# Performance work log

Measured on AMD Instinct MI355X. Metric: run time of the kernel, lower is better.

Reference implementation:

```python
import jax, jax.numpy as jnp
import numpy as np

CONV_KERNEL_MAX_DIFF = 0.7  # self.conv_kernel_max_diff
PRE_KERNEL_MULT = 1.0       # self.pre_conv_kernel_mult


def setup_inputs() -> dict:
    B, C, N, K = 8, 64, 32, 3
    key = jax.random.key(0)
    k1, k2, k3 = jax.random.split(key, 3)
    conv_in = jax.random.normal(k1, (B, C, N, N), dtype=jnp.float32)
    pre_kernel = jax.random.normal(k2, (B, C, C, K, K), dtype=jnp.float32)
    bias = jax.random.normal(k3, (B, C, 1, 1), dtype=jnp.float32)
    return {"conv_in": conv_in, "pre_kernel": pre_kernel, "bias": bias}


def _identity_kernel(c, k, dtype):
    # 1 at the spatial center for matching in/out channel -> identity circular conv
    idx = jnp.arange(c)
    return jnp.zeros((c, c, k, k), dtype=dtype).at[idx, idx, k // 2, k // 2].set(1.0)


def reference(conv_in, pre_kernel, bias):
    B, C, N, _ = conv_in.shape
    Kk = pre_kernel.shape[-1]
    # K = 0.7 * tanh(pre_kernel) + I
    Kmat = CONV_KERNEL_MAX_DIFF * jnp.tanh(PRE_KERNEL_MULT * pre_kernel)
    Kmat = Kmat + _identity_kernel(C, Kk, conv_in.dtype)[None]
    # Embed k x k kernel into n x n with the center tap at the origin
    # (so the identity kernel acts as the identity map under circular conv).
    Kpad = jnp.zeros((B, C, C, N, N), dtype=conv_in.dtype).at[..., :Kk, :Kk].set(Kmat)
    Kpad = jnp.roll(Kpad, shift=(-(Kk // 2), -(Kk // 2)), axis=(-2, -1))
    # Circular conv2D diagonalizes per-frequency into c x c complex matrices.
    K_hat = jnp.fft.fft2(Kpad)            # [B,C,C,N,N] complex
    x_hat = jnp.fft.fft2(conv_in)         # [B,C,N,N] complex
    y_hat = jnp.einsum('boiuv,biuv->bouv', K_hat, x_hat)
    conv_out = jnp.real(jnp.fft.ifft2(y_hat)) + bias
    # log|det| of the block-circulant operator = sum over frequencies of
    # log|det K_hat[:, :, u, v]| (Schur-complement recursion in the original).
    mats = jnp.transpose(K_hat, (0, 3, 4, 1, 2))  # [B,N,N,C,C]
    _, logabsdet = jnp.linalg.slogdet(mats)
    logdet = jnp.sum(logabsdet, axis=(1, 2))      # [B]
    return conv_out, logdet
```

## Files before the change

kernel.cpp:

```cpp
#include <hip/hip_runtime.h>
#include <math.h>

#define BB 8
#define CC 64
#define NN 32
#define CONV_TOTAL (BB*CC*NN*NN)
#define KM_ELEMS (BB*9*CC*CC)
#define NCANON 514

typedef float v2f __attribute__((ext_vector_type(2)));

#define RL(x, l) __uint_as_float(__builtin_amdgcn_readlane(__float_as_uint(x), (l)))

__global__ __launch_bounds__(256) void build_km(const float* __restrict__ pre,
                                                float* __restrict__ km,
                                                float* __restrict__ logdet_out) {
    int idx = blockIdx.x * 256 + threadIdx.x;
    if (blockIdx.x == 0 && threadIdx.x < BB) logdet_out[threadIdx.x] = 0.f;
    if (idx >= KM_ELEMS) return;
    int b   = idx / (9 * 4096);
    int rem = idx - b * (9 * 4096);
    int j   = rem >> 12;
    int e   = rem & 4095;
    int o = e >> 6, i = e & 63;
    float v = 0.7f * tanhf(pre[(b * 4096 + e) * 9 + j]);
    if (o == i && j == 4) v += 1.0f;
    km[idx] = v;
}

__global__ __launch_bounds__(256) void conv_kernel(const float* __restrict__ x,
                                                   const float* __restrict__ km,
                                                   const float* __restrict__ bias,
                                                   float* __restrict__ out) {
    int b = blockIdx.x >> 6, o = blockIdx.x & 63;
    __shared__ float Kms[9][64];
    __shared__ float xs[1024];
    int t = threadIdx.x;
    for (int s = t; s < 576; s += 256) {
        int j = s >> 6, i = s & 63;
        Kms[j][i] = km[(b * 9 + j) * 4096 + (o << 6) + i];
    }
    float bb = bias[(b << 6) + o];
    float acc0 = bb, acc1 = bb, acc2 = bb, acc3 = bb;
    int u = t >> 3, v0 = (t & 7) << 2;
    const float* xb = x + (size_t)(b << 6) * 1024;
    for (int i = 0; i < 64; ++i) {
        float4 xv4 = *(const float4*)(xb + i * 1024 + (t << 2));
        __syncthreads();
        *(float4*)&xs[t << 2] = xv4;
        __syncthreads();
        #pragma unroll
        for (int dy = 0; dy < 3; ++dy) {
            int row = (u + 1 - dy) & 31;
            const float* xr = &xs[row << 5];
            float xv[6];
            #pragma unroll
            for (int q = 0; q < 6; ++q) xv[q] = xr[(v0 - 1 + q) & 31];
            #pragma unroll
            for (int dx = 0; dx < 3; ++dx) {
                float w = Kms[dy * 3 + dx][i];
                acc0 += w * xv[2 - dx];
                acc1 += w * xv[3 - dx];
                acc2 += w * xv[4 - dx];
                acc3 += w * xv[5 - dx];
            }
        }
    }
    float4 r = make_float4(acc0, acc1, acc2, acc3);
    *(float4*)(out + ((size_t)blockIdx.x << 10) + (u << 5) + v0) = r;
}

template<int K>
__device__ __forceinline__ void lu_steps(v2f (&A)[64], int lane, float &logsum) {
    float px = RL(A[K].x, K), py = RL(A[K].y, K);
    float mag = fmaf(px, px, py * py);
    logsum += 0.5f * __logf(mag);
    if constexpr (K < 63) {
        float inv = __builtin_amdgcn_rcpf(mag);
        float ax = A[K].x, ay = A[K].y;
        float mr = (ax * px + ay * py) * inv;
        float mi = (ay * px - ax * py) * inv;
        bool act = lane > K;
        mr = act ? mr : 0.f;
        mi = act ? mi : 0.f;
        v2f m1 = (v2f){-mr, -mr};
        v2f m2 = (v2f){ mi, -mi};
        #pragma unroll
        for (int c = K + 1; c < 64; ++c) {
            float pcx = RL(A[c].x, K), pcy = RL(A[c].y, K);
            v2f p1 = (v2f){pcx, pcy};
            v2f p2 = (v2f){pcy, pcx};
            A[c] = m1 * p1 + A[c];
            A[c] = m2 * p2 + A[c];
        }
        lu_steps<K + 1>(A, lane, logsum);
    }
}

__global__ __launch_bounds__(64, 1) void logdet_kernel(const float* __restrict__ km,
                                                       float* __restrict__ logdet_out) {
    int gid = blockIdx.x;
    int b = gid / NCANON, ci = gid - b * NCANON;
    int u, v;
    if (ci < 17)        { u = 0;                  v = ci; }
    else if (ci < 497)  { int r = ci - 17; u = 1 + (r >> 5); v = r & 31; }
    else                { u = 16;                 v = ci - 497; }
    float wgt = ((u == 0 || u == 16) && (v == 0 || v == 16)) ? 1.0f : 2.0f;

    int lane = threadIdx.x;

    v2f A[64];
    #pragma unroll
    for (int c = 0; c < 64; ++c) A[c] = (v2f){0.f, 0.f};

    const float* Kb = km + (size_t)b * 36864 + (lane << 6);
    #pragma unroll
    for (int j = 0; j < 9; ++j) {
        int dy = j / 3, dx = j % 3;
        float argrev = -(float)(u * (dy - 1) + v * (dx - 1)) * (1.0f / 32.0f);
        argrev = argrev - floorf(argrev);
        float cs = __builtin_amdgcn_cosf(argrev);
        float sn = __builtin_amdgcn_sinf(argrev);
        v2f csn = (v2f){cs, sn};
        const float* p = Kb + (j << 12);
        #pragma unroll
        for (int ch = 0; ch < 8; ++ch) {
            float4 k0 = *(const float4*)(p + (ch << 3) + 0);
            float4 k1 = *(const float4*)(p + (ch << 3) + 4);
            A[(ch << 3) + 0] += csn * k0.x;  A[(ch << 3) + 1] += csn * k0.y;
            A[(ch << 3) + 2] += csn * k0.z;  A[(ch << 3) + 3] += csn * k0.w;
            A[(ch << 3) + 4] += csn * k1.x;  A[(ch << 3) + 5] += csn * k1.y;
            A[(ch << 3) + 6] += csn * k1.z;  A[(ch << 3) + 7] += csn * k1.w;
            __builtin_amdgcn_sched_barrier(0);
        }
    }

    float logsum = 0.f;
    lu_steps<0>(A, lane, logsum);

    if (lane == 0) atomicAdd(&logdet_out[b], wgt * logsum);
}

extern "C" void kernel_launch(void* const* d_in, const int* in_sizes, int n_in,
                              void* d_out, int out_size, void* d_ws, size_t ws_size,
                              hipStream_t stream) {
    const float* conv_in    = (const float*)d_in[0];
    const float* pre_kernel = (const float*)d_in[1];
    const float* bias       = (const float*)d_in[2];
    float* out = (float*)d_out;
    float* km  = (float*)d_ws;
    float* logdet_out = out + CONV_TOTAL;

    build_km<<<KM_ELEMS / 256, 256, 0, stream>>>(pre_kernel, km, logdet_out);
    conv_kernel<<<BB * CC, 256, 0, stream>>>(conv_in, km, bias, out);
    logdet_kernel<<<BB * NCANON, 64, 0, stream>>>(km, logdet_out);
}
```

Baseline: 223.3 us.

## Split per-frequency LU across two waves with shared-memory multiplier exchange

The logdet kernel now uses 128 threads per block, with each wave holding 32 of the 64 complex columns in an interleaved groups-of-four layout. The wave that owns the pivot column computes the multipliers, shares them through a double-buffered LDS array, and both waves update their columns after a block barrier. This halves per-thread register pressure and the serial elimination work per wave, allowing more occupancy. The cost is 63 __syncthreads plus LDS traffic per matrix.

```diff
diff --git a/kernel.cpp b/kernel.cpp
--- a/kernel.cpp
+++ b/kernel.cpp
@@ -70,35 +70,61 @@
     *(float4*)(out + ((size_t)blockIdx.x << 10) + (u << 5) + v0) = r;
 }
 
+
+constexpr int cnt_le(int K, int w) {
+    int G = (K + 1) >> 3, rem = (K + 1) & 7;
+    int part = rem - 4 * w;
+    part = part < 0 ? 0 : (part > 4 ? 4 : part);
+    return G * 4 + part;
+}
+
 template<int K>
-__device__ __forceinline__ void lu_steps(v2f (&A)[64], int lane, float &logsum) {
-    float px = RL(A[K].x, K), py = RL(A[K].y, K);
-    float mag = fmaf(px, px, py * py);
-    logsum += 0.5f * __logf(mag);
+__device__ __forceinline__ void lu_steps(v2f (&A)[32], int wave, int lane,
+                                         float &lsum, v2f (*mbuf)[64]) {
+    constexpr int WK = (K >> 2) & 1;
+    constexpr int IK = ((K >> 3) << 2) + (K & 3);
+    if (wave == WK) {
+        float px = RL(A[IK].x, K), py = RL(A[IK].y, K);
+        float mag = fmaf(px, px, py * py);
+        lsum += 0.5f * __logf(mag);
+        if constexpr (K < 63) {
+            float inv = __builtin_amdgcn_rcpf(mag);
+            float ax = A[IK].x, ay = A[IK].y;
+            float mr = (ax * px + ay * py) * inv;
+            float mi = (ay * px - ax * py) * inv;
+            bool act = lane > K;
+            v2f m;
+            m.x = act ? mr : 0.f;
+            m.y = act ? mi : 0.f;
+            mbuf[K & 1][lane] = m;
+        }
+    }
     if constexpr (K < 63) {
-        float inv = __builtin_amdgcn_rcpf(mag);
-        float ax = A[K].x, ay = A[K].y;
-        float mr = (ax * px + ay * py) * inv;
-        float mi = (ay * px - ax * py) * inv;
-        bool act = lane > K;
-        mr = act ? mr : 0.f;
-        mi = act ? mi : 0.f;
-        v2f m1 = (v2f){-mr, -mr};
-        v2f m2 = (v2f){ mi, -mi};
-        #pragma unroll
-        for (int c = K + 1; c < 64; ++c) {
-            float pcx = RL(A[c].x, K), pcy = RL(A[c].y, K);
-            v2f p1 = (v2f){pcx, pcy};
-            v2f p2 = (v2f){pcy, pcx};
-            A[c] = m1 * p1 + A[c];
-            A[c] = m2 * p2 + A[c];
+        __syncthreads();
+        v2f m = mbuf[K & 1][lane];
+        if (wave == 0) {
+            constexpr int I0 = cnt_le(K, 0);
+            #pragma unroll
+            for (int i = I0; i < 32; ++i) {
+                float pcx = RL(A[i].x, K), pcy = RL(A[i].y, K);
+                A[i].x = fmaf(-m.x, pcx, fmaf( m.y, pcy, A[i].x));
+                A[i].y = fmaf(-m.x, pcy, fmaf(-m.y, pcx, A[i].y));
+            }
+        } else {
+            constexpr int I0 = cnt_le(K, 1);
+            #pragma unroll
+            for (int i = I0; i < 32; ++i) {
+                float pcx = RL(A[i].x, K), pcy = RL(A[i].y, K);
+                A[i].x = fmaf(-m.x, pcx, fmaf( m.y, pcy, A[i].x));
+                A[i].y = fmaf(-m.x, pcy, fmaf(-m.y, pcx, A[i].y));
+            }
         }
-        lu_steps<K + 1>(A, lane, logsum);
+        lu_steps<K + 1>(A, wave, lane, lsum, mbuf);
     }
 }
 
-__global__ __launch_bounds__(64, 1) void logdet_kernel(const float* __restrict__ km,
-                                                       float* __restrict__ logdet_out) {
+__global__ __launch_bounds__(128, 4) void logdet_kernel(const float* __restrict__ km,
+                                                        float* __restrict__ logdet_out) {
     int gid = blockIdx.x;
     int b = gid / NCANON, ci = gid - b * NCANON;
     int u, v;
@@ -107,13 +133,16 @@
     else                { u = 16;                 v = ci - 497; }
     float wgt = ((u == 0 || u == 16) && (v == 0 || v == 16)) ? 1.0f : 2.0f;
 
-    int lane = threadIdx.x;
+    int tid  = threadIdx.x;
+    int wave = tid >> 6, lane = tid & 63;
 
-    v2f A[64];
+    __shared__ v2f mbuf[2][64];
+
+    v2f A[32];
     #pragma unroll
-    for (int c = 0; c < 64; ++c) A[c] = (v2f){0.f, 0.f};
+    for (int i = 0; i < 32; ++i) A[i] = (v2f){0.f, 0.f};
 
-    const float* Kb = km + (size_t)b * 36864 + (lane << 6);
+    const float* Kb = km + (size_t)b * 36864 + (lane << 6) + (wave << 2);
     #pragma unroll
     for (int j = 0; j < 9; ++j) {
         int dy = j / 3, dx = j % 3;
@@ -124,21 +153,20 @@
         v2f csn = (v2f){cs, sn};
         const float* p = Kb + (j << 12);
         #pragma unroll
-        for (int ch = 0; ch < 8; ++ch) {
-            float4 k0 = *(const float4*)(p + (ch << 3) + 0);
-            float4 k1 = *(const float4*)(p + (ch << 3) + 4);
-            A[(ch << 3) + 0] += csn * k0.x;  A[(ch << 3) + 1] += csn * k0.y;
-            A[(ch << 3) + 2] += csn * k0.z;  A[(ch << 3) + 3] += csn * k0.w;
-            A[(ch << 3) + 4] += csn * k1.x;  A[(ch << 3) + 5] += csn * k1.y;
-            A[(ch << 3) + 6] += csn * k1.z;  A[(ch << 3) + 7] += csn * k1.w;
-            __builtin_amdgcn_sched_barrier(0);
+        for (int q = 0; q < 8; ++q) {
+            float4 k4 = *(const float4*)(p + (q << 3));
+            A[(q << 2) + 0] += csn * k4.x;
+            A[(q << 2) + 1] += csn * k4.y;
+            A[(q << 2) + 2] += csn * k4.z;
+            A[(q << 2) + 3] += csn * k4.w;
+            if ((q & 3) == 3) __builtin_amdgcn_sched_barrier(0);
         }
     }
 
-    float logsum = 0.f;
-    lu_steps<0>(A, lane, logsum);
+    float lsum = 0.f;
+    lu_steps<0>(A, wave, lane, lsum, mbuf);
 
-    if (lane == 0) atomicAdd(&logdet_out[b], wgt * logsum);
+    if (lane == 0) atomicAdd(&logdet_out[b], wgt * lsum);
 }
 
 extern "C" void kernel_launch(void* const* d_in, const int* in_sizes, int n_in,
@@ -153,5 +181,5 @@
 
     build_km<<<KM_ELEMS / 256, 256, 0, stream>>>(pre_kernel, km, logdet_out);
     conv_kernel<<<BB * CC, 256, 0, stream>>>(conv_in, km, bias, out);
-    logdet_kernel<<<BB * NCANON, 64, 0, stream>>>(km, logdet_out);
+    logdet_kernel<<<BB * NCANON, 128, 0, stream>>>(km, logdet_out);
 }
```

Measured after the change: 397.4 us. 1.78x slower.
